# Performance work log

Measured on AMD Instinct MI355X. Metric: run time of the kernel, lower is better.

The kernel has to match this reference:

```python
import jax, jax.numpy as jnp
import numpy as np

B, T, D, H, O, E = 2, 2048, 1024, 4096, 1024, 8


def setup_inputs() -> dict:
    key = jax.random.key(0)
    ks = jax.random.split(key, 8)
    s = lambda fan_in: 1.0 / np.sqrt(fan_in)
    return {
        "x": jax.random.normal(ks[0], (B, T, D), dtype=jnp.float32),
        "Wg": jax.random.uniform(ks[1], (D, E), minval=-s(D), maxval=s(D)),
        "bg": jax.random.uniform(ks[2], (E,), minval=-s(D), maxval=s(D)),
        "W1": jax.random.uniform(ks[3], (E, D, H), minval=-s(D), maxval=s(D)),
        "b1": jax.random.uniform(ks[4], (E, H), minval=-s(D), maxval=s(D)),
        "W2": jax.random.uniform(ks[5], (E, H, O), minval=-s(H), maxval=s(H)),
        "b2": jax.random.uniform(ks[6], (E, O), minval=-s(H), maxval=s(H)),
        "num_experts_per_tok": 2,
    }


def reference(x, Wg, bg, W1, b1, W2, b2, num_experts_per_tok):
    # gating: softmax over experts  [B,T,E]
    scores = jax.nn.softmax(jnp.einsum('btd,de->bte', x, Wg) + bg, axis=-1)
    # top-k mask (scatter of ones at topk indices)
    _, idx = jax.lax.top_k(scores, num_experts_per_tok)          # [B,T,k]
    mask = jax.nn.one_hot(idx, E, dtype=scores.dtype).sum(axis=-2)  # [B,T,E]
    gated = scores * mask
    # F.normalize(p=1): divide by L1 norm clamped to eps
    gated = gated / jnp.maximum(jnp.sum(jnp.abs(gated), axis=-1, keepdims=True), 1e-12)
    # all experts run on all tokens (naive MoE)
    hidden = jax.nn.relu(jnp.einsum('btd,edh->beth', x, W1) + b1[None, :, None, :])  # [B,E,T,H]
    expert_out = jnp.einsum('beth,eho->beto', hidden, W2) + b2[None, :, None, :]     # [B,E,T,O]
    # combine: einsum('bte,bteo->bto') with expert_outputs transposed(1,2)
    return jnp.einsum('bte,beto->bto', gated, expert_out)
```

## Files before the change

kernel.cpp:

```cpp
#include <hip/hip_runtime.h>
#include <hip/hip_bf16.h>
#include <cstdio>

#define NT_TOK 4096
#define D_DIM  1024
#define H_DIM  4096
#define O_DIM  1024
#define E_NUM  8
#define PAIRS  8192
#define WI_SLOTS 72
#define BK 64
#define G1_BLOCKS (32 * WI_SLOTS)
#define TW1_BLOCKS (E_NUM * 1024)
#define TW2_BLOCKS (E_NUM * 1024)

typedef short bf16x8 __attribute__((ext_vector_type(8)));
typedef float f32x4  __attribute__((ext_vector_type(4)));

__device__ __forceinline__ unsigned short bfr(float f){
  unsigned u = __float_as_uint(f);
  unsigned r = (u + 0x7FFFu + ((u >> 16) & 1u)) >> 16;
  return (unsigned short)r;
}

__device__ __forceinline__ void gload_lds16(const void* g, void* l){
  __builtin_amdgcn_global_load_lds((const __attribute__((address_space(1))) unsigned int*)g,
                                   (__attribute__((address_space(3))) unsigned int*)l,
                                   16, 0, 0);
}

__device__ __forceinline__ void transpose_tile(const float* __restrict__ in,
                                               unsigned short* __restrict__ out,
                                               int R, int C, int bx, int by, int bz,
                                               char* smem){
  float (*t)[65] = (float(*)[65])smem;
  long long base = (long long)bz * R * C;
  int c0 = bx * 64, r0 = by * 64;
  int tid = threadIdx.x;
  int rr = tid >> 4;
  int cc = (tid & 15) * 4;
  #pragma unroll
  for (int i = 0; i < 4; i++){
    int r = rr + i * 16;
    float4 v = *(const float4*)&in[base + (long long)(r0 + r) * C + c0 + cc];
    t[r][cc] = v.x; t[r][cc+1] = v.y; t[r][cc+2] = v.z; t[r][cc+3] = v.w;
  }
  __syncthreads();
  #pragma unroll
  for (int i = 0; i < 4; i++){
    int oc = rr + i * 16;
    unsigned int lo = (unsigned int)bfr(t[cc][oc])   | ((unsigned int)bfr(t[cc+1][oc]) << 16);
    unsigned int hi = (unsigned int)bfr(t[cc+2][oc]) | ((unsigned int)bfr(t[cc+3][oc]) << 16);
    *(uint2*)&out[base + (long long)(c0 + oc) * R + r0 + cc] = make_uint2(lo, hi);
  }
}

__global__ __launch_bounds__(256) void gate_w1t_kernel(const float* __restrict__ x,
                                                       const float* __restrict__ Wg,
                                                       const float* __restrict__ bg,
                                                       const float* __restrict__ W1,
                                                       unsigned short* __restrict__ xb,
                                                       unsigned short* __restrict__ W1t,
                                                       int*   __restrict__ pe,
                                                       float* __restrict__ pw,
                                                       int*   __restrict__ chist){
  __shared__ __align__(16) char smem[16640];
  int bid = blockIdx.x;
  if (bid >= NT_TOK/4){
    int tb = bid - NT_TOK/4;
    int e = tb >> 10, t = tb & 1023;
    transpose_tile(W1, W1t, D_DIM, H_DIM, t & 63, t >> 6, e, smem);
    return;
  }
  int wid = threadIdx.x >> 6, lane = threadIdx.x & 63;
  int t = bid * 4 + wid;
  const float* xr = x + (long long)t * D_DIM;
  unsigned short* xo = xb + (long long)t * D_DIM;
  float acc[E_NUM];
  #pragma unroll
  for (int e = 0; e < E_NUM; e++) acc[e] = 0.f;
  for (int d = lane; d < D_DIM; d += 64){
    float xv = xr[d];
    xo[d] = bfr(xv);
    const float* wr = Wg + d * E_NUM;
    #pragma unroll
    for (int e = 0; e < E_NUM; e++) acc[e] += xv * wr[e];
  }
  #pragma unroll
  for (int off = 32; off; off >>= 1)
    #pragma unroll
    for (int e = 0; e < E_NUM; e++) acc[e] += __shfl_xor(acc[e], off);
  if (lane == 0){
    float l[E_NUM];
    float m = -1e30f;
    #pragma unroll
    for (int e = 0; e < E_NUM; e++){ l[e] = acc[e] + bg[e]; m = fmaxf(m, l[e]); }
    float ex[E_NUM];
    #pragma unroll
    for (int e = 0; e < E_NUM; e++) ex[e] = expf(l[e] - m);
    int e0 = 0;
    #pragma unroll
    for (int e = 1; e < E_NUM; e++) if (ex[e] > ex[e0]) e0 = e;
    int e1 = -1;
    for (int e = 0; e < E_NUM; e++){ if (e == e0) continue; if (e1 < 0 || ex[e] > ex[e1]) e1 = e; }
    float s = ex[e0] + ex[e1];
    pe[2*t]   = e0;  pw[2*t]   = ex[e0] / s;
    pe[2*t+1] = e1;  pw[2*t+1] = ex[e1] / s;
    int chunk = (2*t) >> 8;
    atomicAdd(&chist[chunk * E_NUM + e0], 1);
    atomicAdd(&chist[chunk * E_NUM + e1], 1);
  }
}

__global__ __launch_bounds__(256) void scatter_kernel(const int* __restrict__ pe,
                                                      const int* __restrict__ chunk_hist,
                                                      int* __restrict__ cnt,
                                                      int* __restrict__ offs,
                                                      int* __restrict__ row_pair,
                                                      int* __restrict__ wi){
  __shared__ int hist[32][E_NUM];
  __shared__ int pref[32][E_NUM];
  __shared__ int total[E_NUM];
  __shared__ int off_s[E_NUM + 1];
  __shared__ unsigned char ex[PAIRS];
  int tid = threadIdx.x;
  for (int i = tid; i < PAIRS; i += 256) ex[i] = (unsigned char)pe[i];
  { int c = tid >> 3, e = tid & 7; hist[c][e] = chunk_hist[tid]; }
  __syncthreads();
  if (tid < E_NUM){
    int s = 0;
    for (int c = 0; c < 32; c++){ pref[c][tid] = s; s += hist[c][tid]; }
    total[tid] = s;
  }
  __syncthreads();
  if (tid == 0){
    int s = 0;
    for (int e = 0; e < E_NUM; e++){ off_s[e] = s; s += total[e]; }
    off_s[E_NUM] = s;
    int idx = 0;
    for (int e = 0; e < E_NUM; e++){
      int mts = (total[e] + 127) >> 7;
      for (int m = 0; m < mts; m++) wi[idx++] = (e << 8) | m;
    }
    for (; idx < WI_SLOTS; idx++) wi[idx] = -1;
  }
  __syncthreads();
  if (tid < E_NUM){ cnt[tid] = total[tid]; offs[tid] = off_s[tid]; }
  int c = tid >> 3, e = tid & 7;
  int base = off_s[e] + pref[c][e];
  int local = 0;
  for (int i = 0; i < 256; i++){
    int p = c * 256 + i;
    if (ex[p] == (unsigned char)e){
      row_pair[base + local] = p;
      local++;
    }
  }
}

__global__ __launch_bounds__(256, 3) void gemm1_w2t_kernel(const unsigned short* __restrict__ xb,
                                                           const unsigned short* __restrict__ W1t,
                                                           const float* __restrict__ W2,
                                                           unsigned short* __restrict__ W2t,
                                                           const float* __restrict__ b1,
                                                           const int* __restrict__ row_pair,
                                                           const int* __restrict__ cnt,
                                                           const int* __restrict__ offs,
                                                           const int* __restrict__ wi,
                                                           unsigned short* __restrict__ hidden){
  __shared__ __align__(16) char smem[32768];
  int bid = blockIdx.x;
  if (bid >= G1_BLOCKS){
    int tb = bid - G1_BLOCKS;
    int e = tb >> 10, t = tb & 1023;
    transpose_tile(W2, W2t, H_DIM, O_DIM, t & 15, t >> 4, e, smem);
    return;
  }
  int nt = bid & 31, slot = bid >> 5;
  int w = wi[slot];
  if (w < 0) return;
  int e = w >> 8, mt = w & 255;
  int count = cnt[e];
  int m0 = mt * 128;
  int seg = offs[e];
  int valid = count - m0;
  int n0 = nt * 128;

  unsigned short* As = (unsigned short*)smem;
  unsigned short* Bs = (unsigned short*)(smem + 16384);

  int tid = threadIdx.x;
  int wv = tid >> 6, lane = tid & 63;
  int wr = wv >> 1, wc = wv & 1;
  int lo = lane & 15, hi = lane >> 4;
  int l3 = lane >> 3;
  int srcel = ((lane & 7) ^ l3) << 3;

  const unsigned short* w1e = W1t + (long long)e * H_DIM * D_DIM;

  const unsigned short* pa[4];
  const unsigned short* pb[4];
  #pragma unroll
  for (int h = 0; h < 4; h++){
    int r = h * 32 + wv * 8 + l3;
    int pos = seg + m0 + r; if (pos > PAIRS - 1) pos = PAIRS - 1;
    int token = row_pair[pos] >> 1;
    pa[h] = xb + (long long)token * D_DIM + srcel;
    pb[h] = w1e + (long long)(n0 + r) * D_DIM + srcel;
  }

  f32x4 acc[4][4] = {};
  for (int kt = 0; kt < D_DIM / BK; ++kt){
    #pragma unroll
    for (int h = 0; h < 4; h++){
      gload_lds16(pa[h], &As[(h*32 + wv*8) * BK]);  pa[h] += BK;
      gload_lds16(pb[h], &Bs[(h*32 + wv*8) * BK]);  pb[h] += BK;
    }
    __syncthreads();
    bf16x8 aq[4][2], bq[4][2];
    #pragma unroll
    for (int n = 0; n < 4; n++)
      #pragma unroll
      for (int ks = 0; ks < 2; ks++){
        int br = wc*64 + n*16 + lo;
        bq[n][ks] = *(const bf16x8*)&Bs[br*BK + ((ks*32 + hi*8) ^ ((br & 7) << 3))];
      }
    #pragma unroll
    for (int m = 0; m < 4; m++)
      #pragma unroll
      for (int ks = 0; ks < 2; ks++){
        int ar = wr*64 + m*16 + lo;
        aq[m][ks] = *(const bf16x8*)&As[ar*BK + ((ks*32 + hi*8) ^ ((ar & 7) << 3))];
      }
    #pragma unroll
    for (int m = 0; m < 4; m++)
      #pragma unroll
      for (int n = 0; n < 4; n++)
        #pragma unroll
        for (int ks = 0; ks < 2; ks++)
          acc[m][n] = __builtin_amdgcn_mfma_f32_16x16x32_bf16(aq[m][ks], bq[n][ks], acc[m][n], 0, 0, 0);
    __syncthreads();
  }

  const float* b1e = b1 + (long long)e * H_DIM;
  #pragma unroll
  for (int n = 0; n < 4; n++){
    int col = n0 + wc*64 + n*16 + lo;
    float bias = b1e[col];
    #pragma unroll
    for (int m = 0; m < 4; m++)
      #pragma unroll
      for (int j = 0; j < 4; j++){
        int rl = wr*64 + m*16 + hi*4 + j;
        if (rl < valid){
          float v = acc[m][n][j] + bias;
          v = v > 0.f ? v : 0.f;
          hidden[(long long)(seg + m0 + rl) * H_DIM + col] = bfr(v);
        }
      }
  }
}

__global__ __launch_bounds__(256, 3) void gemm2_kernel(const unsigned short* __restrict__ hidden,
                                                       const unsigned short* __restrict__ W2t,
                                                       const float* __restrict__ b2,
                                                       const int* __restrict__ row_pair,
                                                       const int* __restrict__ cnt,
                                                       const int* __restrict__ offs,
                                                       const int* __restrict__ wi,
                                                       float* __restrict__ y){
  int w = wi[blockIdx.y];
  if (w < 0) return;
  int e = w >> 8, mt = w & 255;
  int nt = blockIdx.x;
  int count = cnt[e];
  int m0 = mt * 128;
  int seg = offs[e];
  int valid = count - m0;
  int n0 = nt * 128;

  __shared__ unsigned short As[128 * BK];
  __shared__ unsigned short Bs[128 * BK];

  int tid = threadIdx.x;
  int wv = tid >> 6, lane = tid & 63;
  int wr = wv >> 1, wc = wv & 1;
  int lo = lane & 15, hi = lane >> 4;
  int l3 = lane >> 3;
  int srcel = ((lane & 7) ^ l3) << 3;

  const unsigned short* w2e = W2t + (long long)e * O_DIM * H_DIM;

  const unsigned short* pa[4];
  const unsigned short* pb[4];
  #pragma unroll
  for (int h = 0; h < 4; h++){
    int r = h * 32 + wv * 8 + l3;
    long long pos = seg + m0 + r; if (pos > PAIRS - 1) pos = PAIRS - 1;
    pa[h] = hidden + pos * H_DIM + srcel;
    pb[h] = w2e + (long long)(n0 + r) * H_DIM + srcel;
  }

  f32x4 acc[4][4] = {};
  for (int kt = 0; kt < H_DIM / BK; ++kt){
    #pragma unroll
    for (int h = 0; h < 4; h++){
      gload_lds16(pa[h], &As[(h*32 + wv*8) * BK]);  pa[h] += BK;
      gload_lds16(pb[h], &Bs[(h*32 + wv*8) * BK]);  pb[h] += BK;
    }
    __syncthreads();
    bf16x8 aq[4][2], bq[4][2];
    #pragma unroll
    for (int n = 0; n < 4; n++)
      #pragma unroll
      for (int ks = 0; ks < 2; ks++){
        int br = wc*64 + n*16 + lo;
        bq[n][ks] = *(const bf16x8*)&Bs[br*BK + ((ks*32 + hi*8) ^ ((br & 7) << 3))];
      }
    #pragma unroll
    for (int m = 0; m < 4; m++)
      #pragma unroll
      for (int ks = 0; ks < 2; ks++){
        int ar = wr*64 + m*16 + lo;
        aq[m][ks] = *(const bf16x8*)&As[ar*BK + ((ks*32 + hi*8) ^ ((ar & 7) << 3))];
      }
    #pragma unroll
    for (int m = 0; m < 4; m++)
      #pragma unroll
      for (int n = 0; n < 4; n++)
        #pragma unroll
        for (int ks = 0; ks < 2; ks++)
          acc[m][n] = __builtin_amdgcn_mfma_f32_16x16x32_bf16(aq[m][ks], bq[n][ks], acc[m][n], 0, 0, 0);
    __syncthreads();
  }

  const float* b2e = b2 + (long long)e * O_DIM;
  #pragma unroll
  for (int m = 0; m < 4; m++)
    #pragma unroll
    for (int j = 0; j < 4; j++){
      int rl = wr*64 + m*16 + hi*4 + j;
      if (rl < valid){
        int p = row_pair[seg + m0 + rl];
        float* yr = y + (long long)p * O_DIM;
        #pragma unroll
        for (int n = 0; n < 4; n++){
          int col = n0 + wc*64 + n*16 + lo;
          yr[col] = acc[m][n][j] + b2e[col];
        }
      }
    }
}

__global__ __launch_bounds__(256) void combine_kernel(const float* __restrict__ y,
                                                      const int* __restrict__ pe,
                                                      const float* __restrict__ pw,
                                                      float* __restrict__ out){
  int t = blockIdx.x, tid = threadIdx.x;
  float w0 = pw[2*t], w1 = pw[2*t+1];
  float4 a = ((const float4*)(y + (long long)(2*t) * O_DIM))[tid];
  float4 b = ((const float4*)(y + (long long)(2*t+1) * O_DIM))[tid];
  float4 r;
  r.x = w0 * a.x + w1 * b.x;
  r.y = w0 * a.y + w1 * b.y;
  r.z = w0 * a.z + w1 * b.z;
  r.w = w0 * a.w + w1 * b.w;
  ((float4*)(out + (long long)t * O_DIM))[tid] = r;
}

extern "C" void kernel_launch(void* const* d_in, const int* in_sizes, int n_in,
                              void* d_out, int out_size, void* d_ws, size_t ws_size,
                              hipStream_t stream){
  const float* x  = (const float*)d_in[0];
  const float* Wg = (const float*)d_in[1];
  const float* bg = (const float*)d_in[2];
  const float* W1 = (const float*)d_in[3];
  const float* b1 = (const float*)d_in[4];
  const float* W2 = (const float*)d_in[5];
  const float* b2 = (const float*)d_in[6];
  float* out = (float*)d_out;

  char* ws = (char*)d_ws;
  size_t off = 0;
  auto alloc = [&](size_t bytes){ size_t r = off; off += (bytes + 255) & ~(size_t)255; return r; };

  unsigned short* W1t    = (unsigned short*)(ws + alloc((size_t)E_NUM * H_DIM * D_DIM * 2));
  unsigned short* W2t    = (unsigned short*)(ws + alloc((size_t)E_NUM * O_DIM * H_DIM * 2));
  unsigned short* xb     = (unsigned short*)(ws + alloc((size_t)NT_TOK * D_DIM * 2));
  unsigned short* hidden = (unsigned short*)(ws + alloc((size_t)PAIRS * H_DIM * 2));
  int*            pe     = (int*)           (ws + alloc(PAIRS * 4));
  float*          pw     = (float*)         (ws + alloc(PAIRS * 4));
  int*            row_pair = (int*)         (ws + alloc(PAIRS * 4));
  int*            cnt    = (int*)           (ws + alloc(64));
  int*            offs   = (int*)           (ws + alloc(64));
  int*            chist  = (int*)           (ws + alloc(32 * E_NUM * 4));
  int*            wi     = (int*)           (ws + alloc(WI_SLOTS * 4));

  float* yp = (float*)W1t;

  if (off > ws_size)
    fprintf(stderr, "kernel_launch: workspace too small: need %zu, have %zu\n", off, ws_size);

  hipMemsetAsync(chist, 0, 32 * E_NUM * 4, stream);
  gate_w1t_kernel<<<NT_TOK/4 + TW1_BLOCKS, 256, 0, stream>>>(x, Wg, bg, W1, xb, W1t, pe, pw, chist);
  scatter_kernel<<<1, 256, 0, stream>>>(pe, chist, cnt, offs, row_pair, wi);
  gemm1_w2t_kernel<<<G1_BLOCKS + TW2_BLOCKS, 256, 0, stream>>>(xb, W1t, W2, W2t, b1,
                                                               row_pair, cnt, offs, wi, hidden);
  gemm2_kernel<<<dim3(O_DIM/128, WI_SLOTS), 256, 0, stream>>>(hidden, W2t, b2, row_pair, cnt, offs, wi, yp);
  combine_kernel<<<NT_TOK, 256, 0, stream>>>(yp, pe, pw, out);
}
```

Before: 324.0 us.

## Use 256-row tiles in gemm1 and fuse combine into gemm2 via atomics

GEMM1 now processes 256 routed rows per block instead of 128, so each W1 tile loaded from memory feeds twice as many rows. A separate 256-row work list is built for it, and LDS grows to 48KB. GEMM2 now scales its output by the gate weight and atomically adds into a zeroed output, which removes the intermediate y buffer and the combine kernel. The costs are higher register and LDS pressure, fewer gemm1 blocks, float atomics with nondeterministic summation order, and an extra memset.

```diff
diff --git a/kernel.cpp b/kernel.cpp
--- a/kernel.cpp
+++ b/kernel.cpp
@@ -8,9 +8,10 @@
 #define O_DIM  1024
 #define E_NUM  8
 #define PAIRS  8192
-#define WI_SLOTS 72
+#define WI128_SLOTS 72
+#define WI256_SLOTS 40
 #define BK 64
-#define G1_BLOCKS (32 * WI_SLOTS)
+#define G1_BLOCKS (32 * WI256_SLOTS)
 #define TW1_BLOCKS (E_NUM * 1024)
 #define TW2_BLOCKS (E_NUM * 1024)
 
@@ -117,7 +118,8 @@
                                                       int* __restrict__ cnt,
                                                       int* __restrict__ offs,
                                                       int* __restrict__ row_pair,
-                                                      int* __restrict__ wi){
+                                                      int* __restrict__ wi128,
+                                                      int* __restrict__ wi256){
   __shared__ int hist[32][E_NUM];
   __shared__ int pref[32][E_NUM];
   __shared__ int total[E_NUM];
@@ -137,12 +139,15 @@
     int s = 0;
     for (int e = 0; e < E_NUM; e++){ off_s[e] = s; s += total[e]; }
     off_s[E_NUM] = s;
-    int idx = 0;
+    int i1 = 0, i2 = 0;
     for (int e = 0; e < E_NUM; e++){
-      int mts = (total[e] + 127) >> 7;
-      for (int m = 0; m < mts; m++) wi[idx++] = (e << 8) | m;
-    }
-    for (; idx < WI_SLOTS; idx++) wi[idx] = -1;
+      int m128 = (total[e] + 127) >> 7;
+      for (int m = 0; m < m128; m++) wi128[i1++] = (e << 8) | m;
+      int m256 = (total[e] + 255) >> 8;
+      for (int m = 0; m < m256; m++) wi256[i2++] = (e << 8) | m;
+    }
+    for (; i1 < WI128_SLOTS; i1++) wi128[i1] = -1;
+    for (; i2 < WI256_SLOTS; i2++) wi256[i2] = -1;
   }
   __syncthreads();
   if (tid < E_NUM){ cnt[tid] = total[tid]; offs[tid] = off_s[tid]; }
@@ -166,9 +171,9 @@
                                                            const int* __restrict__ row_pair,
                                                            const int* __restrict__ cnt,
                                                            const int* __restrict__ offs,
-                                                           const int* __restrict__ wi,
+                                                           const int* __restrict__ wi256,
                                                            unsigned short* __restrict__ hidden){
-  __shared__ __align__(16) char smem[32768];
+  __shared__ __align__(16) char smem[49152];
   int bid = blockIdx.x;
   if (bid >= G1_BLOCKS){
     int tb = bid - G1_BLOCKS;
@@ -176,18 +181,18 @@
     transpose_tile(W2, W2t, H_DIM, O_DIM, t & 15, t >> 4, e, smem);
     return;
   }
-  int nt = bid & 31, slot = bid >> 5;
-  int w = wi[slot];
+  int slot = bid >> 5, nt = bid & 31;
+  int w = wi256[slot];
   if (w < 0) return;
   int e = w >> 8, mt = w & 255;
   int count = cnt[e];
-  int m0 = mt * 128;
+  int m0 = mt * 256;
   int seg = offs[e];
   int valid = count - m0;
   int n0 = nt * 128;
 
   unsigned short* As = (unsigned short*)smem;
-  unsigned short* Bs = (unsigned short*)(smem + 16384);
+  unsigned short* Bs = (unsigned short*)(smem + 32768);
 
   int tid = threadIdx.x;
   int wv = tid >> 6, lane = tid & 63;
@@ -198,26 +203,33 @@
 
   const unsigned short* w1e = W1t + (long long)e * H_DIM * D_DIM;
 
-  const unsigned short* pa[4];
+  const unsigned short* pa[8];
   const unsigned short* pb[4];
   #pragma unroll
-  for (int h = 0; h < 4; h++){
+  for (int h = 0; h < 8; h++){
     int r = h * 32 + wv * 8 + l3;
     int pos = seg + m0 + r; if (pos > PAIRS - 1) pos = PAIRS - 1;
     int token = row_pair[pos] >> 1;
     pa[h] = xb + (long long)token * D_DIM + srcel;
+  }
+  #pragma unroll
+  for (int h = 0; h < 4; h++){
+    int r = h * 32 + wv * 8 + l3;
     pb[h] = w1e + (long long)(n0 + r) * D_DIM + srcel;
   }
 
-  f32x4 acc[4][4] = {};
+  f32x4 acc[8][4] = {};
   for (int kt = 0; kt < D_DIM / BK; ++kt){
     #pragma unroll
+    for (int h = 0; h < 8; h++){
+      gload_lds16(pa[h], &As[(h*32 + wv*8) * BK]);  pa[h] += BK;
+    }
+    #pragma unroll
     for (int h = 0; h < 4; h++){
-      gload_lds16(pa[h], &As[(h*32 + wv*8) * BK]);  pa[h] += BK;
       gload_lds16(pb[h], &Bs[(h*32 + wv*8) * BK]);  pb[h] += BK;
     }
     __syncthreads();
-    bf16x8 aq[4][2], bq[4][2];
+    bf16x8 bq[4][2];
     #pragma unroll
     for (int n = 0; n < 4; n++)
       #pragma unroll
@@ -226,19 +238,23 @@
         bq[n][ks] = *(const bf16x8*)&Bs[br*BK + ((ks*32 + hi*8) ^ ((br & 7) << 3))];
       }
     #pragma unroll
-    for (int m = 0; m < 4; m++)
-      #pragma unroll
-      for (int ks = 0; ks < 2; ks++){
-        int ar = wr*64 + m*16 + lo;
-        aq[m][ks] = *(const bf16x8*)&As[ar*BK + ((ks*32 + hi*8) ^ ((ar & 7) << 3))];
-      }
-    #pragma unroll
-    for (int m = 0; m < 4; m++)
-      #pragma unroll
-      for (int n = 0; n < 4; n++)
+    for (int mh = 0; mh < 2; mh++){
+      bf16x8 aq[4][2];
+      #pragma unroll
+      for (int i = 0; i < 4; i++)
         #pragma unroll
-        for (int ks = 0; ks < 2; ks++)
-          acc[m][n] = __builtin_amdgcn_mfma_f32_16x16x32_bf16(aq[m][ks], bq[n][ks], acc[m][n], 0, 0, 0);
+        for (int ks = 0; ks < 2; ks++){
+          int ar = wr*128 + (mh*4 + i)*16 + lo;
+          aq[i][ks] = *(const bf16x8*)&As[ar*BK + ((ks*32 + hi*8) ^ ((ar & 7) << 3))];
+        }
+      #pragma unroll
+      for (int i = 0; i < 4; i++)
+        #pragma unroll
+        for (int n = 0; n < 4; n++)
+          #pragma unroll
+          for (int ks = 0; ks < 2; ks++)
+            acc[mh*4+i][n] = __builtin_amdgcn_mfma_f32_16x16x32_bf16(aq[i][ks], bq[n][ks], acc[mh*4+i][n], 0, 0, 0);
+    }
     __syncthreads();
   }
 
@@ -248,10 +264,10 @@
     int col = n0 + wc*64 + n*16 + lo;
     float bias = b1e[col];
     #pragma unroll
-    for (int m = 0; m < 4; m++)
+    for (int m = 0; m < 8; m++)
       #pragma unroll
       for (int j = 0; j < 4; j++){
-        int rl = wr*64 + m*16 + hi*4 + j;
+        int rl = wr*128 + m*16 + hi*4 + j;
         if (rl < valid){
           float v = acc[m][n][j] + bias;
           v = v > 0.f ? v : 0.f;
@@ -267,9 +283,10 @@
                                                        const int* __restrict__ row_pair,
                                                        const int* __restrict__ cnt,
                                                        const int* __restrict__ offs,
-                                                       const int* __restrict__ wi,
-                                                       float* __restrict__ y){
-  int w = wi[blockIdx.y];
+                                                       const int* __restrict__ wi128,
+                                                       const float* __restrict__ pw,
+                                                       float* __restrict__ out){
+  int w = wi128[blockIdx.y];
   if (w < 0) return;
   int e = w >> 8, mt = w & 255;
   int nt = blockIdx.x;
@@ -342,30 +359,15 @@
       int rl = wr*64 + m*16 + hi*4 + j;
       if (rl < valid){
         int p = row_pair[seg + m0 + rl];
-        float* yr = y + (long long)p * O_DIM;
+        float wgt = pw[p];
+        float* orow = out + (long long)(p >> 1) * O_DIM;
         #pragma unroll
         for (int n = 0; n < 4; n++){
           int col = n0 + wc*64 + n*16 + lo;
-          yr[col] = acc[m][n][j] + b2e[col];
+          atomicAdd(&orow[col], wgt * (acc[m][n][j] + b2e[col]));
         }
       }
     }
-}
-
-__global__ __launch_bounds__(256) void combine_kernel(const float* __restrict__ y,
-                                                      const int* __restrict__ pe,
-                                                      const float* __restrict__ pw,
-                                                      float* __restrict__ out){
-  int t = blockIdx.x, tid = threadIdx.x;
-  float w0 = pw[2*t], w1 = pw[2*t+1];
-  float4 a = ((const float4*)(y + (long long)(2*t) * O_DIM))[tid];
-  float4 b = ((const float4*)(y + (long long)(2*t+1) * O_DIM))[tid];
-  float4 r;
-  r.x = w0 * a.x + w1 * b.x;
-  r.y = w0 * a.y + w1 * b.y;
-  r.z = w0 * a.z + w1 * b.z;
-  r.w = w0 * a.w + w1 * b.w;
-  ((float4*)(out + (long long)t * O_DIM))[tid] = r;
 }
 
 extern "C" void kernel_launch(void* const* d_in, const int* in_sizes, int n_in,
@@ -394,18 +396,18 @@
   int*            cnt    = (int*)           (ws + alloc(64));
   int*            offs   = (int*)           (ws + alloc(64));
   int*            chist  = (int*)           (ws + alloc(32 * E_NUM * 4));
-  int*            wi     = (int*)           (ws + alloc(WI_SLOTS * 4));
-
-  float* yp = (float*)W1t;
+  int*            wi128  = (int*)           (ws + alloc(WI128_SLOTS * 4));
+  int*            wi256  = (int*)           (ws + alloc(WI256_SLOTS * 4));
 
   if (off > ws_size)
     fprintf(stderr, "kernel_launch: workspace too small: need %zu, have %zu\n", off, ws_size);
 
   hipMemsetAsync(chist, 0, 32 * E_NUM * 4, stream);
+  hipMemsetAsync(out, 0, (size_t)NT_TOK * O_DIM * 4, stream);
   gate_w1t_kernel<<<NT_TOK/4 + TW1_BLOCKS, 256, 0, stream>>>(x, Wg, bg, W1, xb, W1t, pe, pw, chist);
-  scatter_kernel<<<1, 256, 0, stream>>>(pe, chist, cnt, offs, row_pair, wi);
+  scatter_kernel<<<1, 256, 0, stream>>>(pe, chist, cnt, offs, row_pair, wi128, wi256);
   gemm1_w2t_kernel<<<G1_BLOCKS + TW2_BLOCKS, 256, 0, stream>>>(xb, W1t, W2, W2t, b1,
-                                                               row_pair, cnt, offs, wi, hidden);
-  gemm2_kernel<<<dim3(O_DIM/128, WI_SLOTS), 256, 0, stream>>>(hidden, W2t, b2, row_pair, cnt, offs, wi, yp);
-  combine_kernel<<<NT_TOK, 256, 0, stream>>>(yp, pe, pw, out);
-}
+                                                               row_pair, cnt, offs, wi256, hidden);
+  gemm2_kernel<<<dim3(O_DIM/128, WI128_SLOTS), 256, 0, stream>>>(hidden, W2t, b2, row_pair, cnt, offs,
+                                                                 wi128, pw, out);
+}
```

Result: slower. 361.1 us (+11.4%).
